# Kernel optimization log

Measured on AMD Instinct MI355X. Metric: run time of the kernel, lower is better.

Reference implementation:

```python
import jax, jax.numpy as jnp
import numpy as np

N_NODES = 50000


def _glorot(key, fan_in, fan_out):
    limit = float(np.sqrt(6.0 / (fan_in + fan_out)))
    return jax.random.uniform(key, (fan_in, fan_out), jnp.float32, -limit, limit)


def setup_inputs() -> dict:
    key = jax.random.key(0)
    k_x, k_src, k_dst, k1, k2, k3 = jax.random.split(key, 6)
    x = jax.random.normal(k_x, (N_NODES, 128), dtype=jnp.float32)
    src = jax.random.randint(k_src, (800000,), 0, N_NODES)
    dst = jax.random.randint(k_dst, (800000,), 0, N_NODES)
    edge_index = jnp.stack([src, dst]).astype(jnp.int64)  # [2, E]
    W1 = _glorot(k1, 128, 96)
    W2 = _glorot(k2, 96, 96)
    W3 = _glorot(k3, 96, 40)
    b1 = jnp.zeros((96,), jnp.float32)
    b2 = jnp.zeros((96,), jnp.float32)
    b3 = jnp.zeros((40,), jnp.float32)
    return {"x": x, "W1": W1, "b1": b1, "W2": W2, "b2": b2,
            "W3": W3, "b3": b3, "edge_index": edge_index}


def _aggregate(x, src, dst):
    # sparse adj SpMM with 'add' reduce: out[dst] += x[src]
    return jax.ops.segment_sum(x[src], dst, num_segments=N_NODES)


def reference(x, W1, b1, W2, b2, W3, b3, edge_index):
    src, dst = edge_index[0], edge_index[1]
    # layer 1: aggregate -> linear -> relu (dropout identity in eval)
    h = jax.nn.relu(_aggregate(x, src, dst) @ W1 + b1)
    # layer 2
    h = jax.nn.relu(_aggregate(h, src, dst) @ W2 + b2)
    # layer 3 + log_softmax
    logits = _aggregate(h, src, dst) @ W3 + b3
    return jax.nn.log_softmax(logits, axis=-1)
```

## Files before the change

### kernel.cpp

```cpp
#include <hip/hip_runtime.h>
#include <math.h>

typedef __attribute__((ext_vector_type(8))) short bf16x8;
typedef __attribute__((ext_vector_type(4))) float f32x4;

__device__ __forceinline__ unsigned short f2bf(float f) {
  unsigned u = __float_as_uint(f);
  u += 0x7fffu + ((u >> 16) & 1u);
  return (unsigned short)(u >> 16);
}
__device__ __forceinline__ float bflo(unsigned u) { return __uint_as_float(u << 16); }
__device__ __forceinline__ float bfhi(unsigned u) { return __uint_as_float(u & 0xffff0000u); }

#define ACC8(U)                                           \
  a0 += bflo(U.x); a1 += bfhi(U.x); a2 += bflo(U.y); a3 += bfhi(U.y); \
  a4 += bflo(U.z); a5 += bfhi(U.z); a6 += bflo(U.w); a7 += bfhi(U.w)


constexpr int EB = 4096;
constexpr int QT = 64;
constexpr int SLOT = 3072;

__device__ __forceinline__ void gemm1_tile(int bx, int tid, const float* __restrict__ x,
                                           const uint4* __restrict__ sW,
                                           unsigned short* __restrict__ Tb, int N) {
  int wid = tid >> 6;
  int lane = tid & 63;
  int rt = bx * 4 + wid;
  if (rt * 16 >= N) return;
  int quad = lane >> 4;
  int lm = lane & 15;
  union BU { uint4 u; bf16x8 v; };
  f32x4 acc[6];
#pragma unroll
  for (int c = 0; c < 6; ++c) acc[c] = (f32x4){0.f, 0.f, 0.f, 0.f};
  int row = rt * 16 + lm;
  if (row >= N) row = N - 1;
#pragma unroll
  for (int s = 0; s < 4; ++s) {
    int k0 = s * 32 + quad * 8;
    const float* Af = x + (size_t)row * 128 + k0;
    float4 x0 = *(const float4*)(Af);
    float4 x1 = *(const float4*)(Af + 4);
    union { unsigned short s[8]; bf16x8 v; } au;
    au.s[0] = f2bf(x0.x); au.s[1] = f2bf(x0.y); au.s[2] = f2bf(x0.z); au.s[3] = f2bf(x0.w);
    au.s[4] = f2bf(x1.x); au.s[5] = f2bf(x1.y); au.s[6] = f2bf(x1.z); au.s[7] = f2bf(x1.w);
#pragma unroll
    for (int c = 0; c < 6; ++c) {
      BU bu;
      bu.u = sW[(s * 6 + c) * 64 + lane];
      acc[c] = __builtin_amdgcn_mfma_f32_16x16x32_bf16(au.v, bu.v, acc[c], 0, 0, 0);
    }
  }
#pragma unroll
  for (int c = 0; c < 6; ++c) {
    int colv = c * 16 + lm;
#pragma unroll
    for (int r = 0; r < 4; ++r) {
      int orow = rt * 16 + quad * 4 + r;
      if (orow < N) Tb[(size_t)orow * 96 + colv] = f2bf(acc[c][r]);
    }
  }
}

struct BinSM {
  int lcnt[512];
  int lstart[512];
  int cur[512];
  int stage[EB];
};
union D1SM {
  BinSM b;
  uint4 sW[1536];
};

__global__ __launch_bounds__(256) void d1_bin_gemm_pack(
    const int* __restrict__ src, const int* __restrict__ dst,
    int* __restrict__ partial, int* __restrict__ packed,
    const float* __restrict__ x, const float* __restrict__ W1,
    const float* __restrict__ W2, const float* __restrict__ W3,
    unsigned short* __restrict__ Wp2, unsigned short* __restrict__ Wp3,
    unsigned short* __restrict__ Tb, int E, int N, int NBv, int NBIN, int GB) {
  __shared__ D1SM sm;
  int tid = threadIdx.x;
  if ((int)blockIdx.x < NBIN) {
    int* lcnt = sm.b.lcnt;
    int* lstart = sm.b.lstart;
    int* cur = sm.b.cur;
    int* stage = sm.b.stage;
    lcnt[tid] = 0;
    lcnt[tid + 256] = 0;
    __syncthreads();
    int E4 = E >> 2;
    int base4 = blockIdx.x * (EB >> 2);
    int sv[16], dv[16];
    int nv = 0;
#pragma unroll
    for (int j = 0; j < 4; ++j) {
      int idx4 = base4 + j * 256 + tid;
      if (idx4 < E4 && idx4 < base4 + (EB >> 2)) {
        int4 s4 = ((const int4*)src)[idx4];
        int4 d4 = ((const int4*)dst)[idx4];
        sv[j * 4 + 0] = s4.x; dv[j * 4 + 0] = d4.x;
        sv[j * 4 + 1] = s4.y; dv[j * 4 + 1] = d4.y;
        sv[j * 4 + 2] = s4.z; dv[j * 4 + 2] = d4.z;
        sv[j * 4 + 3] = s4.w; dv[j * 4 + 3] = d4.w;
        nv = j * 4 + 4;
      }
    }
#pragma unroll
    for (int i = 0; i < 16; ++i)
      if (i < nv) atomicAdd(&lcnt[dv[i] >> 7], 1);
    bool last = ((int)blockIdx.x == NBIN - 1);
    int tl = E & 3;
    if (last && tid == 0)
      for (int t = 0; t < tl; ++t) atomicAdd(&lcnt[dst[E4 * 4 + t] >> 7], 1);
    __syncthreads();
    lstart[tid] = lcnt[tid];
    lstart[tid + 256] = lcnt[tid + 256];
    __syncthreads();
    for (int off = 1; off < 512; off <<= 1) {
      int a0 = (tid >= off) ? lstart[tid - off] : 0;
      int i1 = tid + 256;
      int a1 = (i1 >= off) ? lstart[i1 - off] : 0;
      __syncthreads();
      lstart[tid] += a0;
      lstart[i1] += a1;
      __syncthreads();
    }
    int e0 = lstart[tid] - lcnt[tid];
    int e1 = lstart[tid + 256] - lcnt[tid + 256];
    __syncthreads();
    lstart[tid] = e0; cur[tid] = e0;
    lstart[tid + 256] = e1; cur[tid + 256] = e1;
    __syncthreads();
#pragma unroll
    for (int i = 0; i < 16; ++i)
      if (i < nv) {
        int b = dv[i] >> 7;
        int p = atomicAdd(&cur[b], 1);
        stage[p] = ((dv[i] & 127) << 16) | (sv[i] & 0xffff);
      }
    if (last && tid == 0)
      for (int t = 0; t < tl; ++t) {
        int d = dst[E4 * 4 + t], s = src[E4 * 4 + t];
        int p = atomicAdd(&cur[d >> 7], 1);
        stage[p] = ((d & 127) << 16) | (s & 0xffff);
      }
    int c0 = lcnt[tid]; if (c0 > QT) c0 = QT;
    int c1 = lcnt[tid + 256]; if (c1 > QT) c1 = QT;
    partial[blockIdx.x * 512 + tid] = c0;
    partial[blockIdx.x * 512 + tid + 256] = c1;
    __syncthreads();
    int meB = lstart[511] + lcnt[511];
    for (int i = tid; i < meB; i += 256) {
      int lo = 0, hi = 511;
      while (lo < hi) {
        int mid = (lo + hi + 1) >> 1;
        if (lstart[mid] <= i) lo = mid; else hi = mid - 1;
      }
      int j = i - lstart[lo];
      if (j < QT) packed[((size_t)blockIdx.x * NBv + lo) * QT + j] = stage[i];
    }
    return;
  }
  int gb = blockIdx.x - NBIN;
  if (gb < GB) {
#pragma unroll
    for (int k = 0; k < 6; ++k) {
      int t = tid + k * 256;
      int lane = t & 63;
      int frag = t >> 6;
      int s = frag / 6;
      int ct = frag - s * 6;
      int colv = ct * 16 + (lane & 15);
      int k0 = s * 32 + (lane >> 4) * 8;
      union { unsigned short h[8]; uint4 u; } pk;
#pragma unroll
      for (int j = 0; j < 8; ++j) pk.h[j] = f2bf(W1[(k0 + j) * 96 + colv]);
      sm.sW[t] = pk.u;
    }
    __syncthreads();
    gemm1_tile(gb, tid, x, sm.sW, Tb, N);
    return;
  }
  int gid = (gb - GB) * 256 + tid;
  const float* W;
  unsigned short* Wp;
  int t, NCTT, M, MV;
  if (gid < 1152) {
    W = W2; Wp = Wp2; t = gid; NCTT = 6; M = 96; MV = 96;
  } else if (gid < 1728) {
    W = W3; Wp = Wp3; t = gid - 1152; NCTT = 3; M = 40; MV = 40;
  } else {
    return;
  }
  int lane = t & 63;
  int frag = t >> 6;
  int s = frag / NCTT;
  int ct = frag - s * NCTT;
  int colv = ct * 16 + (lane & 15);
  int k0 = s * 32 + (lane >> 4) * 8;
  union { unsigned short h[8]; uint4 u; } pk;
#pragma unroll
  for (int j = 0; j < 8; ++j) {
    float v = (colv < MV) ? W[(k0 + j) * M + colv] : 0.f;
    pk.h[j] = f2bf(v);
  }
  ((uint4*)Wp)[t] = pk.u;
}

__global__ __launch_bounds__(256) void build_csr(const int* __restrict__ partial,
                                                 const int* __restrict__ packed,
                                                 int* __restrict__ row_ptr,
                                                 int* __restrict__ degA,
                                                 int* __restrict__ col, int N, int NBv,
                                                 int NBIN) {
  __shared__ int e[257];
  __shared__ int stage[SLOT];
  __shared__ int cnt[128];
  __shared__ int sm2[128];
  __shared__ int dsv[128];
  int tid = threadIdx.x;
  int b = blockIdx.x;
  int c = (tid < NBIN) ? partial[tid * 512 + b] : 0;
  e[tid] = c;
  __syncthreads();
  for (int off = 1; off < 256; off <<= 1) {
    int a = (tid >= off) ? e[tid - off] : 0;
    __syncthreads();
    e[tid] += a;
    __syncthreads();
  }
  int excl = e[tid] - c;
  __syncthreads();
  e[tid] = excl;
  if (tid == 255) e[256] = excl + c;
  __syncthreads();
  int me = e[256];
  if (me > SLOT) me = SLOT;
  for (int i = tid; i < me; i += 256) {
    int lo = 0, hi = 255;
    while (lo < hi) {
      int mid = (lo + hi + 1) >> 1;
      if (e[mid] <= i) lo = mid; else hi = mid - 1;
    }
    stage[i] = packed[((size_t)lo * NBv + b) * QT + (i - e[lo])];
  }
  if (tid < 128) cnt[tid] = 0;
  __syncthreads();
  for (int i = tid; i < me; i += 256) atomicAdd(&cnt[stage[i] >> 16], 1);
  __syncthreads();
  int node0 = b << 7;
  int RL = N - node0;
  if (RL > 128) RL = 128;
  if (tid < 128) {
    sm2[tid] = cnt[tid];
    dsv[tid] = cnt[tid];
  }
  __syncthreads();
  for (int off = 1; off < 128; off <<= 1) {
    int u = (tid >= off && tid < 128) ? sm2[tid - off] : 0;
    __syncthreads();
    if (tid < 128) sm2[tid] += u;
    __syncthreads();
  }
  if (tid < 128) {
    int ex2 = b * SLOT + sm2[tid] - dsv[tid];
    cnt[tid] = ex2;
    if (tid < RL) {
      row_ptr[node0 + tid] = ex2;
      degA[node0 + tid] = dsv[tid];
    }
  }
  __syncthreads();
  for (int i = tid; i < me; i += 256) {
    int pk = stage[i];
    int p = atomicAdd(&cnt[pk >> 16], 1);
    col[p] = pk & 0xffff;
  }
}


template <int NCT, int MOUT, int MVALID>
__global__ __launch_bounds__(256, 8) void fused_agg_gemm(
    const unsigned short* __restrict__ tin, const int* __restrict__ row_ptr,
    const int* __restrict__ degA, const int* __restrict__ col,
    const float* __restrict__ bias, const unsigned short* __restrict__ Wp,
    unsigned short* __restrict__ outp, int N) {
  constexpr int LST = 104;
  constexpr int CAP = 1536;
  __shared__ unsigned short sH[64 * LST];
  __shared__ int scol[CAP];
  __shared__ int srp[64];
  __shared__ int sdeg[64];
  __shared__ short sperm[64];
  int tid = threadIdx.x;
  int node0 = blockIdx.x * 64;
  int nloc = N - node0;
  if (nloc > 64) nloc = 64;
  if (tid < nloc) srp[tid] = row_ptr[node0 + tid];
  if (tid < 64) sdeg[tid] = (tid < nloc) ? degA[node0 + tid] : 0x7fffffff;
  __syncthreads();
  int gs = srp[0];
  int me = srp[nloc - 1] + sdeg[nloc - 1] - gs;
  for (int i = tid; i < me && i < CAP; i += 256) scol[i] = col[gs + i];
  if (tid < 64) {
    int ki = sdeg[tid];
    int rank = 0;
#pragma unroll 8
    for (int j = 0; j < 64; ++j) {
      int kj = sdeg[j];
      rank += (kj < ki) || (kj == ki && j < tid);
    }
    sperm[rank] = (short)tid;
  }
  __syncthreads();
  bool fits = (me <= CAP);

#pragma unroll
  for (int it = 0; it < 3; ++it) {
    int u = tid + it * 256;
    int sl = u / 12;
    int c = u - sl * 12;
    int nl = sperm[sl];
    if (nl < nloc) {
      int beg = srp[nl] - gs;
      int end = beg + sdeg[nl];
      const unsigned short* tc = tin + 8 * c;
      float a0 = 0.f, a1 = 0.f, a2 = 0.f, a3 = 0.f, a4 = 0.f, a5 = 0.f, a6 = 0.f, a7 = 0.f;
      if (fits) {
        int e = beg;
        for (; e + 3 < end; e += 4) {
          int s0 = scol[e], s1 = scol[e + 1], s2 = scol[e + 2], s3 = scol[e + 3];
          uint4 u0 = *(const uint4*)(tc + (size_t)s0 * 96);
          uint4 u1 = *(const uint4*)(tc + (size_t)s1 * 96);
          uint4 u2 = *(const uint4*)(tc + (size_t)s2 * 96);
          uint4 u3 = *(const uint4*)(tc + (size_t)s3 * 96);
          ACC8(u0); ACC8(u1); ACC8(u2); ACC8(u3);
        }
        for (; e < end; ++e) {
          int s0 = scol[e];
          uint4 u4 = *(const uint4*)(tc + (size_t)s0 * 96);
          ACC8(u4);
        }
      } else {
        for (int e = beg; e < end; ++e) {
          int s0 = col[gs + e];
          uint4 u4 = *(const uint4*)(tc + (size_t)s0 * 96);
          ACC8(u4);
        }
      }
      const float* b = bias + 8 * c;
      union { unsigned short s[8]; uint4 u; } pk;
      pk.s[0] = f2bf(fmaxf(a0 + b[0], 0.f));
      pk.s[1] = f2bf(fmaxf(a1 + b[1], 0.f));
      pk.s[2] = f2bf(fmaxf(a2 + b[2], 0.f));
      pk.s[3] = f2bf(fmaxf(a3 + b[3], 0.f));
      pk.s[4] = f2bf(fmaxf(a4 + b[4], 0.f));
      pk.s[5] = f2bf(fmaxf(a5 + b[5], 0.f));
      pk.s[6] = f2bf(fmaxf(a6 + b[6], 0.f));
      pk.s[7] = f2bf(fmaxf(a7 + b[7], 0.f));
      *(uint4*)&sH[sl * LST + c * 8] = pk.u;
    }
  }
  __syncthreads();

  int wid = tid >> 6;
  int lane = tid & 63;
  int rt16 = wid * 16;
  if (rt16 >= nloc) return;
  int quad = lane >> 4;
  int lm = lane & 15;
  union BU { uint4 u; bf16x8 v; };
  f32x4 acc[NCT];
#pragma unroll
  for (int c = 0; c < NCT; ++c) acc[c] = (f32x4){0.f, 0.f, 0.f, 0.f};
  const uint4* wp4 = (const uint4*)Wp;
#pragma unroll
  for (int s = 0; s < 3; ++s) {
    BU au;
    au.u = *(const uint4*)&sH[(rt16 + lm) * LST + s * 32 + quad * 8];
#pragma unroll
    for (int c = 0; c < NCT; ++c) {
      BU bu;
      bu.u = wp4[(s * NCT + c) * 64 + lane];
      acc[c] = __builtin_amdgcn_mfma_f32_16x16x32_bf16(au.v, bu.v, acc[c], 0, 0, 0);
    }
  }
#pragma unroll
  for (int c = 0; c < NCT; ++c) {
    int colv = c * 16 + lm;
    if (colv >= MVALID) continue;
#pragma unroll
    for (int r = 0; r < 4; ++r) {
      int nl_o = sperm[rt16 + quad * 4 + r];
      if (nl_o < nloc) outp[(size_t)(node0 + nl_o) * MOUT + colv] = f2bf(acc[c][r]);
    }
  }
}

__global__ __launch_bounds__(256) void agg_lsm_bf16(const unsigned short* __restrict__ t,
                                                    const int* __restrict__ row_ptr,
                                                    const int* __restrict__ degA,
                                                    const int* __restrict__ col,
                                                    const float* __restrict__ bias,
                                                    float* __restrict__ out, int N) {
  constexpr int CAPL = 1024;
  __shared__ int scol[CAPL];
  __shared__ int srp[16];
  __shared__ int sdeg[16];
  __shared__ short sperm[16];
  int tid = threadIdx.x;
  int node0 = blockIdx.x * 16;
  int nloc = N - node0;
  if (nloc > 16) nloc = 16;
  if (tid < nloc) srp[tid] = row_ptr[node0 + tid];
  if (tid < 16) sdeg[tid] = (tid < nloc) ? degA[node0 + tid] : 0x7fffffff;
  __syncthreads();
  int gs = srp[0];
  int me = srp[nloc - 1] + sdeg[nloc - 1] - gs;
  for (int i = tid; i < me && i < CAPL; i += 256) scol[i] = col[gs + i];
  if (tid < 16) {
    int ki = sdeg[tid];
    int rank = 0;
#pragma unroll
    for (int j = 0; j < 16; ++j) {
      int kj = sdeg[j];
      rank += (kj < ki) || (kj == ki && j < tid);
    }
    sperm[rank] = (short)tid;
  }
  __syncthreads();
  bool fits = (me <= CAPL);

  int sl = tid >> 4;
  int c = tid & 15;
  int nl = sperm[sl];
  bool act = (c < 10) && (nl < nloc);
  int ceff = (c < 10) ? c : 0;
  const unsigned short* tc = t + 4 * ceff;
  float v0 = 0.f, v1 = 0.f, v2 = 0.f, v3 = 0.f;
  if (act) {
    int beg = srp[nl] - gs;
    int end = beg + sdeg[nl];
    if (fits) {
      int e = beg;
      for (; e + 3 < end; e += 4) {
        int s0 = scol[e], s1 = scol[e + 1], s2 = scol[e + 2], s3 = scol[e + 3];
        uint2 u = *(const uint2*)(tc + (size_t)s0 * 64);
        uint2 w = *(const uint2*)(tc + (size_t)s1 * 64);
        uint2 y = *(const uint2*)(tc + (size_t)s2 * 64);
        uint2 z = *(const uint2*)(tc + (size_t)s3 * 64);
        v0 += bflo(u.x); v1 += bfhi(u.x); v2 += bflo(u.y); v3 += bfhi(u.y);
        v0 += bflo(w.x); v1 += bfhi(w.x); v2 += bflo(w.y); v3 += bfhi(w.y);
        v0 += bflo(y.x); v1 += bfhi(y.x); v2 += bflo(y.y); v3 += bfhi(y.y);
        v0 += bflo(z.x); v1 += bfhi(z.x); v2 += bflo(z.y); v3 += bfhi(z.y);
      }
      for (; e < end; ++e) {
        int s0 = scol[e];
        uint2 u = *(const uint2*)(tc + (size_t)s0 * 64);
        v0 += bflo(u.x); v1 += bfhi(u.x); v2 += bflo(u.y); v3 += bfhi(u.y);
      }
    } else {
      for (int e = beg; e < end; ++e) {
        int s0 = col[gs + e];
        uint2 u = *(const uint2*)(tc + (size_t)s0 * 64);
        v0 += bflo(u.x); v1 += bfhi(u.x); v2 += bflo(u.y); v3 += bfhi(u.y);
      }
    }
  }
  const float* bb = bias + 4 * ceff;
  v0 += bb[0]; v1 += bb[1]; v2 += bb[2]; v3 += bb[3];
  float m = act ? fmaxf(fmaxf(v0, v1), fmaxf(v2, v3)) : -__builtin_inff();
#pragma unroll
  for (int off = 8; off; off >>= 1) m = fmaxf(m, __shfl_xor(m, off, 64));
  float ex = act ? (__expf(v0 - m) + __expf(v1 - m) + __expf(v2 - m) + __expf(v3 - m)) : 0.f;
#pragma unroll
  for (int off = 8; off; off >>= 1) ex += __shfl_xor(ex, off, 64);
  if (act) {
    int node = node0 + nl;
    float l = m + __logf(ex);
    float* o = out + (size_t)node * 40 + 4 * c;
    o[0] = v0 - l; o[1] = v1 - l; o[2] = v2 - l; o[3] = v3 - l;
  }
}


extern "C" void kernel_launch(void* const* d_in, const int* in_sizes, int n_in,
                              void* d_out, int out_size, void* d_ws, size_t ws_size,
                              hipStream_t stream) {
  const float* x  = (const float*)d_in[0];
  const float* W1 = (const float*)d_in[1];
  const float* b1 = (const float*)d_in[2];
  const float* W2 = (const float*)d_in[3];
  const float* b2 = (const float*)d_in[4];
  const float* W3 = (const float*)d_in[5];
  const float* b3 = (const float*)d_in[6];
  const int* edge = (const int*)d_in[7];

  int N = in_sizes[0] / 128;
  int E = in_sizes[7] / 2;
  const int* srcp = edge;
  const int* dstp = edge + E;

  char* p = (char*)d_ws;
  auto alloc = [&](size_t bytes) {
    char* r = p;
    p += (bytes + 255) & ~size_t(255);
    return r;
  };
  int NB = (N + 127) >> 7;
  int NBIN = (E + EB - 1) / EB;
  int GB = ((N + 15) / 16 + 3) / 4;
  int PB = 7;
  int FB = (N + 63) / 64;

  int* partial = (int*)alloc((size_t)NBIN * 512 * 4);
  int* packed  = (int*)alloc((size_t)NBIN * NB * QT * 4);
  int* row_ptr = (int*)alloc((size_t)N * 4);
  int* degA    = (int*)alloc((size_t)N * 4);
  int* col     = (int*)alloc((size_t)NB * SLOT * 4);
  unsigned short* Wp2 = (unsigned short*)alloc(1152 * 8 * 2);
  unsigned short* Wp3 = (unsigned short*)alloc(576 * 8 * 2);
  unsigned short* Tb  = (unsigned short*)alloc((size_t)N * 96 * 2);
  unsigned short* T2b = (unsigned short*)alloc((size_t)N * 96 * 2);
  unsigned short* T3b = (unsigned short*)alloc((size_t)N * 64 * 2);

  d1_bin_gemm_pack<<<NBIN + GB + PB, 256, 0, stream>>>(srcp, dstp, partial, packed,
                                                       x, W1, W2, W3, Wp2, Wp3, Tb,
                                                       E, N, NB, NBIN, GB);
  build_csr<<<NB, 256, 0, stream>>>(partial, packed, row_ptr, degA, col, N, NB, NBIN);
  fused_agg_gemm<6, 96, 96><<<FB, 256, 0, stream>>>(Tb, row_ptr, degA, col, b1, Wp2, T2b, N);
  fused_agg_gemm<3, 64, 40><<<FB, 256, 0, stream>>>(T2b, row_ptr, degA, col, b2, Wp3, T3b, N);
  agg_lsm_bf16<<<(N + 15) / 16, 256, 0, stream>>>(T3b, row_ptr, degA, col, b3, (float*)d_out, N);
}
```

Before: 185.2 us.

## Fuse all GNN stages into one persistent cooperative kernel with grid syncs

```diff
diff --git a/kernel.cpp b/kernel.cpp
--- a/kernel.cpp
+++ b/kernel.cpp
@@ -1,4 +1,5 @@
 #include <hip/hip_runtime.h>
+#include <hip/hip_cooperative_groups.h>
 #include <math.h>
 
 typedef __attribute__((ext_vector_type(8))) short bf16x8;
@@ -20,10 +21,111 @@
 constexpr int EB = 4096;
 constexpr int QT = 64;
 constexpr int SLOT = 3072;
-
-__device__ __forceinline__ void gemm1_tile(int bx, int tid, const float* __restrict__ x,
-                                           const uint4* __restrict__ sW,
-                                           unsigned short* __restrict__ Tb, int N) {
+constexpr int PB = 7;
+
+struct P {
+  const int* src; const int* dst;
+  int* partial; int* packed;
+  const float* x; const float* W1; const float* W2; const float* W3;
+  unsigned short* Wp2; unsigned short* Wp3;
+  unsigned short* Tb; unsigned short* T2b; unsigned short* T3b;
+  int* row_ptr; int* degA; int* col;
+  const float* b1; const float* b2; const float* b3;
+  float* out;
+  int E, N, NB, NBIN, GB, FB, LB;
+};
+
+struct BinSM { int lcnt[512]; int lstart[512]; int cur[512]; int stage[EB]; };
+struct CsrSM { int e[257]; int stage[SLOT]; int cnt[128]; int sm2[128]; int dsv[128]; };
+struct FusedSM {
+  unsigned short sH[64 * 104];
+  int scol[1536];
+  int srp[64]; int sdeg[64]; short sperm[64];
+};
+struct LsmSM { int scol[1024]; int srp[16]; int sdeg[16]; short sperm[16]; };
+union MegaSM { BinSM b; uint4 sW[1536]; CsrSM c; FusedSM f; LsmSM l; };
+
+__device__ void bin_body(const P& p, BinSM& s, int blk, int tid) {
+  int* lcnt = s.lcnt; int* lstart = s.lstart; int* cur = s.cur; int* stage = s.stage;
+  lcnt[tid] = 0;
+  lcnt[tid + 256] = 0;
+  __syncthreads();
+  int E4 = p.E >> 2;
+  int base4 = blk * (EB >> 2);
+  int sv[16], dv[16];
+  int nv = 0;
+#pragma unroll
+  for (int j = 0; j < 4; ++j) {
+    int idx4 = base4 + j * 256 + tid;
+    if (idx4 < E4 && idx4 < base4 + (EB >> 2)) {
+      int4 s4 = ((const int4*)p.src)[idx4];
+      int4 d4 = ((const int4*)p.dst)[idx4];
+      sv[j * 4 + 0] = s4.x; dv[j * 4 + 0] = d4.x;
+      sv[j * 4 + 1] = s4.y; dv[j * 4 + 1] = d4.y;
+      sv[j * 4 + 2] = s4.z; dv[j * 4 + 2] = d4.z;
+      sv[j * 4 + 3] = s4.w; dv[j * 4 + 3] = d4.w;
+      nv = j * 4 + 4;
+    }
+  }
+#pragma unroll
+  for (int i = 0; i < 16; ++i)
+    if (i < nv) atomicAdd(&lcnt[dv[i] >> 7], 1);
+  bool last = (blk == p.NBIN - 1);
+  int tl = p.E & 3;
+  if (last && tid == 0)
+    for (int t = 0; t < tl; ++t) atomicAdd(&lcnt[p.dst[E4 * 4 + t] >> 7], 1);
+  __syncthreads();
+  lstart[tid] = lcnt[tid];
+  lstart[tid + 256] = lcnt[tid + 256];
+  __syncthreads();
+  for (int off = 1; off < 512; off <<= 1) {
+    int a0 = (tid >= off) ? lstart[tid - off] : 0;
+    int i1 = tid + 256;
+    int a1 = (i1 >= off) ? lstart[i1 - off] : 0;
+    __syncthreads();
+    lstart[tid] += a0;
+    lstart[i1] += a1;
+    __syncthreads();
+  }
+  int e0 = lstart[tid] - lcnt[tid];
+  int e1 = lstart[tid + 256] - lcnt[tid + 256];
+  __syncthreads();
+  lstart[tid] = e0; cur[tid] = e0;
+  lstart[tid + 256] = e1; cur[tid + 256] = e1;
+  __syncthreads();
+#pragma unroll
+  for (int i = 0; i < 16; ++i)
+    if (i < nv) {
+      int b = dv[i] >> 7;
+      int pp = atomicAdd(&cur[b], 1);
+      stage[pp] = ((dv[i] & 127) << 16) | (sv[i] & 0xffff);
+    }
+  if (last && tid == 0)
+    for (int t = 0; t < tl; ++t) {
+      int d = p.dst[E4 * 4 + t], ss = p.src[E4 * 4 + t];
+      int pp = atomicAdd(&cur[d >> 7], 1);
+      stage[pp] = ((d & 127) << 16) | (ss & 0xffff);
+    }
+  int c0 = lcnt[tid]; if (c0 > QT) c0 = QT;
+  int c1 = lcnt[tid + 256]; if (c1 > QT) c1 = QT;
+  p.partial[blk * 512 + tid] = c0;
+  p.partial[blk * 512 + tid + 256] = c1;
+  __syncthreads();
+  int meB = lstart[511] + lcnt[511];
+  for (int i = tid; i < meB; i += 256) {
+    int lo = 0, hi = 511;
+    while (lo < hi) {
+      int mid = (lo + hi + 1) >> 1;
+      if (lstart[mid] <= i) lo = mid; else hi = mid - 1;
+    }
+    int j = i - lstart[lo];
+    if (j < QT) p.packed[((size_t)blk * p.NB + lo) * QT + j] = stage[i];
+  }
+}
+
+__device__ void gemm1_tile(int bx, int tid, const float* __restrict__ x,
+                           const uint4* __restrict__ sW,
+                           unsigned short* __restrict__ Tb, int N) {
   int wid = tid >> 6;
   int lane = tid & 63;
   int rt = bx * 4 + wid;
@@ -63,135 +165,34 @@
   }
 }
 
-struct BinSM {
-  int lcnt[512];
-  int lstart[512];
-  int cur[512];
-  int stage[EB];
-};
-union D1SM {
-  BinSM b;
-  uint4 sW[1536];
-};
-
-__global__ __launch_bounds__(256) void d1_bin_gemm_pack(
-    const int* __restrict__ src, const int* __restrict__ dst,
-    int* __restrict__ partial, int* __restrict__ packed,
-    const float* __restrict__ x, const float* __restrict__ W1,
-    const float* __restrict__ W2, const float* __restrict__ W3,
-    unsigned short* __restrict__ Wp2, unsigned short* __restrict__ Wp3,
-    unsigned short* __restrict__ Tb, int E, int N, int NBv, int NBIN, int GB) {
-  __shared__ D1SM sm;
-  int tid = threadIdx.x;
-  if ((int)blockIdx.x < NBIN) {
-    int* lcnt = sm.b.lcnt;
-    int* lstart = sm.b.lstart;
-    int* cur = sm.b.cur;
-    int* stage = sm.b.stage;
-    lcnt[tid] = 0;
-    lcnt[tid + 256] = 0;
-    __syncthreads();
-    int E4 = E >> 2;
-    int base4 = blockIdx.x * (EB >> 2);
-    int sv[16], dv[16];
-    int nv = 0;
-#pragma unroll
-    for (int j = 0; j < 4; ++j) {
-      int idx4 = base4 + j * 256 + tid;
-      if (idx4 < E4 && idx4 < base4 + (EB >> 2)) {
-        int4 s4 = ((const int4*)src)[idx4];
-        int4 d4 = ((const int4*)dst)[idx4];
-        sv[j * 4 + 0] = s4.x; dv[j * 4 + 0] = d4.x;
-        sv[j * 4 + 1] = s4.y; dv[j * 4 + 1] = d4.y;
-        sv[j * 4 + 2] = s4.z; dv[j * 4 + 2] = d4.z;
-        sv[j * 4 + 3] = s4.w; dv[j * 4 + 3] = d4.w;
-        nv = j * 4 + 4;
-      }
-    }
-#pragma unroll
-    for (int i = 0; i < 16; ++i)
-      if (i < nv) atomicAdd(&lcnt[dv[i] >> 7], 1);
-    bool last = ((int)blockIdx.x == NBIN - 1);
-    int tl = E & 3;
-    if (last && tid == 0)
-      for (int t = 0; t < tl; ++t) atomicAdd(&lcnt[dst[E4 * 4 + t] >> 7], 1);
-    __syncthreads();
-    lstart[tid] = lcnt[tid];
-    lstart[tid + 256] = lcnt[tid + 256];
-    __syncthreads();
-    for (int off = 1; off < 512; off <<= 1) {
-      int a0 = (tid >= off) ? lstart[tid - off] : 0;
-      int i1 = tid + 256;
-      int a1 = (i1 >= off) ? lstart[i1 - off] : 0;
-      __syncthreads();
-      lstart[tid] += a0;
-      lstart[i1] += a1;
-      __syncthreads();
-    }
-    int e0 = lstart[tid] - lcnt[tid];
-    int e1 = lstart[tid + 256] - lcnt[tid + 256];
-    __syncthreads();
-    lstart[tid] = e0; cur[tid] = e0;
-    lstart[tid + 256] = e1; cur[tid + 256] = e1;
-    __syncthreads();
-#pragma unroll
-    for (int i = 0; i < 16; ++i)
-      if (i < nv) {
-        int b = dv[i] >> 7;
-        int p = atomicAdd(&cur[b], 1);
-        stage[p] = ((dv[i] & 127) << 16) | (sv[i] & 0xffff);
-      }
-    if (last && tid == 0)
-      for (int t = 0; t < tl; ++t) {
-        int d = dst[E4 * 4 + t], s = src[E4 * 4 + t];
-        int p = atomicAdd(&cur[d >> 7], 1);
-        stage[p] = ((d & 127) << 16) | (s & 0xffff);
-      }
-    int c0 = lcnt[tid]; if (c0 > QT) c0 = QT;
-    int c1 = lcnt[tid + 256]; if (c1 > QT) c1 = QT;
-    partial[blockIdx.x * 512 + tid] = c0;
-    partial[blockIdx.x * 512 + tid + 256] = c1;
-    __syncthreads();
-    int meB = lstart[511] + lcnt[511];
-    for (int i = tid; i < meB; i += 256) {
-      int lo = 0, hi = 511;
-      while (lo < hi) {
-        int mid = (lo + hi + 1) >> 1;
-        if (lstart[mid] <= i) lo = mid; else hi = mid - 1;
-      }
-      int j = i - lstart[lo];
-      if (j < QT) packed[((size_t)blockIdx.x * NBv + lo) * QT + j] = stage[i];
-    }
-    return;
-  }
-  int gb = blockIdx.x - NBIN;
-  if (gb < GB) {
-#pragma unroll
-    for (int k = 0; k < 6; ++k) {
-      int t = tid + k * 256;
-      int lane = t & 63;
-      int frag = t >> 6;
-      int s = frag / 6;
-      int ct = frag - s * 6;
-      int colv = ct * 16 + (lane & 15);
-      int k0 = s * 32 + (lane >> 4) * 8;
-      union { unsigned short h[8]; uint4 u; } pk;
-#pragma unroll
-      for (int j = 0; j < 8; ++j) pk.h[j] = f2bf(W1[(k0 + j) * 96 + colv]);
-      sm.sW[t] = pk.u;
-    }
-    __syncthreads();
-    gemm1_tile(gb, tid, x, sm.sW, Tb, N);
-    return;
-  }
-  int gid = (gb - GB) * 256 + tid;
+__device__ void gemm_body(const P& p, uint4* sW, int gb, int tid) {
+#pragma unroll
+  for (int k = 0; k < 6; ++k) {
+    int t = tid + k * 256;
+    int lane = t & 63;
+    int frag = t >> 6;
+    int s = frag / 6;
+    int ct = frag - s * 6;
+    int colv = ct * 16 + (lane & 15);
+    int k0 = s * 32 + (lane >> 4) * 8;
+    union { unsigned short h[8]; uint4 u; } pk;
+#pragma unroll
+    for (int j = 0; j < 8; ++j) pk.h[j] = f2bf(p.W1[(k0 + j) * 96 + colv]);
+    sW[t] = pk.u;
+  }
+  __syncthreads();
+  gemm1_tile(gb, tid, p.x, sW, p.Tb, p.N);
+}
+
+__device__ void pack_body(const P& p, int pb, int tid) {
+  int gid = pb * 256 + tid;
   const float* W;
   unsigned short* Wp;
   int t, NCTT, M, MV;
   if (gid < 1152) {
-    W = W2; Wp = Wp2; t = gid; NCTT = 6; M = 96; MV = 96;
+    W = p.W2; Wp = p.Wp2; t = gid; NCTT = 6; M = 96; MV = 96;
   } else if (gid < 1728) {
-    W = W3; Wp = Wp3; t = gid - 1152; NCTT = 3; M = 40; MV = 40;
+    W = p.W3; Wp = p.Wp3; t = gid - 1152; NCTT = 3; M = 40; MV = 40;
   } else {
     return;
   }
@@ -210,110 +211,92 @@
   ((uint4*)Wp)[t] = pk.u;
 }
 
-__global__ __launch_bounds__(256) void build_csr(const int* __restrict__ partial,
-                                                 const int* __restrict__ packed,
-                                                 int* __restrict__ row_ptr,
-                                                 int* __restrict__ degA,
-                                                 int* __restrict__ col, int N, int NBv,
-                                                 int NBIN) {
-  __shared__ int e[257];
-  __shared__ int stage[SLOT];
-  __shared__ int cnt[128];
-  __shared__ int sm2[128];
-  __shared__ int dsv[128];
-  int tid = threadIdx.x;
-  int b = blockIdx.x;
-  int c = (tid < NBIN) ? partial[tid * 512 + b] : 0;
-  e[tid] = c;
+__device__ void csr_body(const P& p, CsrSM& s, int b, int tid) {
+  int c = (tid < p.NBIN) ? p.partial[tid * 512 + b] : 0;
+  s.e[tid] = c;
   __syncthreads();
   for (int off = 1; off < 256; off <<= 1) {
-    int a = (tid >= off) ? e[tid - off] : 0;
-    __syncthreads();
-    e[tid] += a;
-    __syncthreads();
-  }
-  int excl = e[tid] - c;
-  __syncthreads();
-  e[tid] = excl;
-  if (tid == 255) e[256] = excl + c;
-  __syncthreads();
-  int me = e[256];
+    int a = (tid >= off) ? s.e[tid - off] : 0;
+    __syncthreads();
+    s.e[tid] += a;
+    __syncthreads();
+  }
+  int excl = s.e[tid] - c;
+  __syncthreads();
+  s.e[tid] = excl;
+  if (tid == 255) s.e[256] = excl + c;
+  __syncthreads();
+  int me = s.e[256];
   if (me > SLOT) me = SLOT;
   for (int i = tid; i < me; i += 256) {
     int lo = 0, hi = 255;
     while (lo < hi) {
       int mid = (lo + hi + 1) >> 1;
-      if (e[mid] <= i) lo = mid; else hi = mid - 1;
-    }
-    stage[i] = packed[((size_t)lo * NBv + b) * QT + (i - e[lo])];
-  }
-  if (tid < 128) cnt[tid] = 0;
-  __syncthreads();
-  for (int i = tid; i < me; i += 256) atomicAdd(&cnt[stage[i] >> 16], 1);
+      if (s.e[mid] <= i) lo = mid; else hi = mid - 1;
+    }
+    s.stage[i] = p.packed[((size_t)lo * p.NB + b) * QT + (i - s.e[lo])];
+  }
+  if (tid < 128) s.cnt[tid] = 0;
+  __syncthreads();
+  for (int i = tid; i < me; i += 256) atomicAdd(&s.cnt[s.stage[i] >> 16], 1);
   __syncthreads();
   int node0 = b << 7;
-  int RL = N - node0;
+  int RL = p.N - node0;
   if (RL > 128) RL = 128;
   if (tid < 128) {
-    sm2[tid] = cnt[tid];
-    dsv[tid] = cnt[tid];
+    s.sm2[tid] = s.cnt[tid];
+    s.dsv[tid] = s.cnt[tid];
   }
   __syncthreads();
   for (int off = 1; off < 128; off <<= 1) {
-    int u = (tid >= off && tid < 128) ? sm2[tid - off] : 0;
-    __syncthreads();
-    if (tid < 128) sm2[tid] += u;
+    int u = (tid >= off && tid < 128) ? s.sm2[tid - off] : 0;
+    __syncthreads();
+    if (tid < 128) s.sm2[tid] += u;
     __syncthreads();
   }
   if (tid < 128) {
-    int ex2 = b * SLOT + sm2[tid] - dsv[tid];
-    cnt[tid] = ex2;
+    int ex2 = b * SLOT + s.sm2[tid] - s.dsv[tid];
+    s.cnt[tid] = ex2;
     if (tid < RL) {
-      row_ptr[node0 + tid] = ex2;
-      degA[node0 + tid] = dsv[tid];
+      p.row_ptr[node0 + tid] = ex2;
+      p.degA[node0 + tid] = s.dsv[tid];
     }
   }
   __syncthreads();
   for (int i = tid; i < me; i += 256) {
-    int pk = stage[i];
-    int p = atomicAdd(&cnt[pk >> 16], 1);
-    col[p] = pk & 0xffff;
-  }
-}
-
+    int pk = s.stage[i];
+    int pos = atomicAdd(&s.cnt[pk >> 16], 1);
+    p.col[pos] = pk & 0xffff;
+  }
+}
 
 template <int NCT, int MOUT, int MVALID>
-__global__ __launch_bounds__(256, 8) void fused_agg_gemm(
-    const unsigned short* __restrict__ tin, const int* __restrict__ row_ptr,
-    const int* __restrict__ degA, const int* __restrict__ col,
-    const float* __restrict__ bias, const unsigned short* __restrict__ Wp,
-    unsigned short* __restrict__ outp, int N) {
+__device__ void fused_body(const unsigned short* __restrict__ tin,
+                           const int* __restrict__ row_ptr, const int* __restrict__ degA,
+                           const int* __restrict__ col, const float* __restrict__ bias,
+                           const unsigned short* __restrict__ Wp,
+                           unsigned short* __restrict__ outp, int N, FusedSM& f,
+                           int item, int tid) {
   constexpr int LST = 104;
   constexpr int CAP = 1536;
-  __shared__ unsigned short sH[64 * LST];
-  __shared__ int scol[CAP];
-  __shared__ int srp[64];
-  __shared__ int sdeg[64];
-  __shared__ short sperm[64];
-  int tid = threadIdx.x;
-  int node0 = blockIdx.x * 64;
+  int node0 = item * 64;
   int nloc = N - node0;
   if (nloc > 64) nloc = 64;
-  if (tid < nloc) srp[tid] = row_ptr[node0 + tid];
-  if (tid < 64) sdeg[tid] = (tid < nloc) ? degA[node0 + tid] : 0x7fffffff;
-  __syncthreads();
-  int gs = srp[0];
-  int me = srp[nloc - 1] + sdeg[nloc - 1] - gs;
-  for (int i = tid; i < me && i < CAP; i += 256) scol[i] = col[gs + i];
+  if (tid < nloc) f.srp[tid] = row_ptr[node0 + tid];
+  if (tid < 64) f.sdeg[tid] = (tid < nloc) ? degA[node0 + tid] : 0x7fffffff;
+  __syncthreads();
+  int gs = f.srp[0];
+  int me = f.srp[nloc - 1] + f.sdeg[nloc - 1] - gs;
+  for (int i = tid; i < me && i < CAP; i += 256) f.scol[i] = col[gs + i];
   if (tid < 64) {
-    int ki = sdeg[tid];
+    int ki = f.sdeg[tid];
     int rank = 0;
 #pragma unroll 8
     for (int j = 0; j < 64; ++j) {
-      int kj = sdeg[j];
+      int kj = f.sdeg[j];
       rank += (kj < ki) || (kj == ki && j < tid);
     }
-    sperm[rank] = (short)tid;
+    f.sperm[rank] = (short)tid;
   }
   __syncthreads();
   bool fits = (me <= CAP);
@@ -323,16 +306,30 @@
     int u = tid + it * 256;
     int sl = u / 12;
     int c = u - sl * 12;
-    int nl = sperm[sl];
+    int nl = f.sperm[sl];
     if (nl < nloc) {
-      int beg = srp[nl] - gs;
-      int end = beg + sdeg[nl];
+      int beg = f.srp[nl] - gs;
+      int end = beg + f.sdeg[nl];
       const unsigned short* tc = tin + 8 * c;
       float a0 = 0.f, a1 = 0.f, a2 = 0.f, a3 = 0.f, a4 = 0.f, a5 = 0.f, a6 = 0.f, a7 = 0.f;
       if (fits) {
         int e = beg;
+        for (; e + 7 < end; e += 8) {
+          int s0 = f.scol[e], s1 = f.scol[e + 1], s2 = f.scol[e + 2], s3 = f.scol[e + 3];
+          int s4 = f.scol[e + 4], s5 = f.scol[e + 5], s6 = f.scol[e + 6], s7 = f.scol[e + 7];
+          uint4 u0 = *(const uint4*)(tc + (size_t)s0 * 96);
+          uint4 u1 = *(const uint4*)(tc + (size_t)s1 * 96);
+          uint4 u2 = *(const uint4*)(tc + (size_t)s2 * 96);
+          uint4 u3 = *(const uint4*)(tc + (size_t)s3 * 96);
+          uint4 u4 = *(const uint4*)(tc + (size_t)s4 * 96);
+          uint4 u5 = *(const uint4*)(tc + (size_t)s5 * 96);
+          uint4 u6 = *(const uint4*)(tc + (size_t)s6 * 96);
+          uint4 u7 = *(const uint4*)(tc + (size_t)s7 * 96);
+          ACC8(u0); ACC8(u1); ACC8(u2); ACC8(u3);
+          ACC8(u4); ACC8(u5); ACC8(u6); ACC8(u7);
+        }
         for (; e + 3 < end; e += 4) {
-          int s0 = scol[e], s1 = scol[e + 1], s2 = scol[e + 2], s3 = scol[e + 3];
+          int s0 = f.scol[e], s1 = f.scol[e + 1], s2 = f.scol[e + 2], s3 = f.scol[e + 3];
           uint4 u0 = *(const uint4*)(tc + (size_t)s0 * 96);
           uint4 u1 = *(const uint4*)(tc + (size_t)s1 * 96);
           uint4 u2 = *(const uint4*)(tc + (size_t)s2 * 96);
@@ -340,15 +337,15 @@
           ACC8(u0); ACC8(u1); ACC8(u2); ACC8(u3);
         }
         for (; e < end; ++e) {
-          int s0 = scol[e];
-          uint4 u4 = *(const uint4*)(tc + (size_t)s0 * 96);
-          ACC8(u4);
+          int s0 = f.scol[e];
+          uint4 u4v = *(const uint4*)(tc + (size_t)s0 * 96);
+          ACC8(u4v);
         }
       } else {
         for (int e = beg; e < end; ++e) {
           int s0 = col[gs + e];
-          uint4 u4 = *(const uint4*)(tc + (size_t)s0 * 96);
-          ACC8(u4);
+          uint4 u4v = *(const uint4*)(tc + (size_t)s0 * 96);
+          ACC8(u4v);
         }
       }
       const float* b = bias + 8 * c;
@@ -361,7 +358,7 @@
       pk.s[5] = f2bf(fmaxf(a5 + b[5], 0.f));
       pk.s[6] = f2bf(fmaxf(a6 + b[6], 0.f));
       pk.s[7] = f2bf(fmaxf(a7 + b[7], 0.f));
-      *(uint4*)&sH[sl * LST + c * 8] = pk.u;
+      *(uint4*)&f.sH[sl * LST + c * 8] = pk.u;
     }
   }
   __syncthreads();
@@ -380,7 +377,7 @@
 #pragma unroll
   for (int s = 0; s < 3; ++s) {
     BU au;
-    au.u = *(const uint4*)&sH[(rt16 + lm) * LST + s * 32 + quad * 8];
+    au.u = *(const uint4*)&f.sH[(rt16 + lm) * LST + s * 32 + quad * 8];
 #pragma unroll
     for (int c = 0; c < NCT; ++c) {
       BU bu;
@@ -394,83 +391,89 @@
     if (colv >= MVALID) continue;
 #pragma unroll
     for (int r = 0; r < 4; ++r) {
-      int nl_o = sperm[rt16 + quad * 4 + r];
+      int nl_o = f.sperm[rt16 + quad * 4 + r];
       if (nl_o < nloc) outp[(size_t)(node0 + nl_o) * MOUT + colv] = f2bf(acc[c][r]);
     }
   }
 }
 
-__global__ __launch_bounds__(256) void agg_lsm_bf16(const unsigned short* __restrict__ t,
-                                                    const int* __restrict__ row_ptr,
-                                                    const int* __restrict__ degA,
-                                                    const int* __restrict__ col,
-                                                    const float* __restrict__ bias,
-                                                    float* __restrict__ out, int N) {
+__device__ void lsm_body(const P& p, LsmSM& L, int item, int tid) {
   constexpr int CAPL = 1024;
-  __shared__ int scol[CAPL];
-  __shared__ int srp[16];
-  __shared__ int sdeg[16];
-  __shared__ short sperm[16];
-  int tid = threadIdx.x;
-  int node0 = blockIdx.x * 16;
-  int nloc = N - node0;
+  const unsigned short* t = p.T3b;
+  int node0 = item * 16;
+  int nloc = p.N - node0;
   if (nloc > 16) nloc = 16;
-  if (tid < nloc) srp[tid] = row_ptr[node0 + tid];
-  if (tid < 16) sdeg[tid] = (tid < nloc) ? degA[node0 + tid] : 0x7fffffff;
-  __syncthreads();
-  int gs = srp[0];
-  int me = srp[nloc - 1] + sdeg[nloc - 1] - gs;
-  for (int i = tid; i < me && i < CAPL; i += 256) scol[i] = col[gs + i];
+  if (tid < nloc) L.srp[tid] = p.row_ptr[node0 + tid];
+  if (tid < 16) L.sdeg[tid] = (tid < nloc) ? p.degA[node0 + tid] : 0x7fffffff;
+  __syncthreads();
+  int gs = L.srp[0];
+  int me = L.srp[nloc - 1] + L.sdeg[nloc - 1] - gs;
+  for (int i = tid; i < me && i < CAPL; i += 256) L.scol[i] = p.col[gs + i];
   if (tid < 16) {
-    int ki = sdeg[tid];
+    int ki = L.sdeg[tid];
     int rank = 0;
 #pragma unroll
     for (int j = 0; j < 16; ++j) {
-      int kj = sdeg[j];
+      int kj = L.sdeg[j];
       rank += (kj < ki) || (kj == ki && j < tid);
     }
-    sperm[rank] = (short)tid;
+    L.sperm[rank] = (short)tid;
   }
   __syncthreads();
   bool fits = (me <= CAPL);
 
   int sl = tid >> 4;
   int c = tid & 15;
-  int nl = sperm[sl];
+  int nl = L.sperm[sl];
   bool act = (c < 10) && (nl < nloc);
   int ceff = (c < 10) ? c : 0;
   const unsigned short* tc = t + 4 * ceff;
   float v0 = 0.f, v1 = 0.f, v2 = 0.f, v3 = 0.f;
   if (act) {
-    int beg = srp[nl] - gs;
-    int end = beg + sdeg[nl];
+    int beg = L.srp[nl] - gs;
+    int end = beg + L.sdeg[nl];
     if (fits) {
       int e = beg;
+      for (; e + 7 < end; e += 8) {
+        uint2 g0 = *(const uint2*)(tc + (size_t)L.scol[e] * 64);
+        uint2 g1 = *(const uint2*)(tc + (size_t)L.scol[e + 1] * 64);
+        uint2 g2 = *(const uint2*)(tc + (size_t)L.scol[e + 2] * 64);
+        uint2 g3 = *(const uint2*)(tc + (size_t)L.scol[e + 3] * 64);
+        uint2 g4 = *(const uint2*)(tc + (size_t)L.scol[e + 4] * 64);
+        uint2 g5 = *(const uint2*)(tc + (size_t)L.scol[e + 5] * 64);
+        uint2 g6 = *(const uint2*)(tc + (size_t)L.scol[e + 6] * 64);
+        uint2 g7 = *(const uint2*)(tc + (size_t)L.scol[e + 7] * 64);
+        v0 += bflo(g0.x); v1 += bfhi(g0.x); v2 += bflo(g0.y); v3 += bfhi(g0.y);
+        v0 += bflo(g1.x); v1 += bfhi(g1.x); v2 += bflo(g1.y); v3 += bfhi(g1.y);
+        v0 += bflo(g2.x); v1 += bfhi(g2.x); v2 += bflo(g2.y); v3 += bfhi(g2.y);
+        v0 += bflo(g3.x); v1 += bfhi(g3.x); v2 += bflo(g3.y); v3 += bfhi(g3.y);
+        v0 += bflo(g4.x); v1 += bfhi(g4.x); v2 += bflo(g4.y); v3 += bfhi(g4.y);
+        v0 += bflo(g5.x); v1 += bfhi(g5.x); v2 += bflo(g5.y); v3 += bfhi(g5.y);
+        v0 += bflo(g6.x); v1 += bfhi(g6.x); v2 += bflo(g6.y); v3 += bfhi(g6.y);
+        v0 += bflo(g7.x); v1 += bfhi(g7.x); v2 += bflo(g7.y); v3 += bfhi(g7.y);
+      }
       for (; e + 3 < end; e += 4) {
-        int s0 = scol[e], s1 = scol[e + 1], s2 = scol[e + 2], s3 = scol[e + 3];
-        uint2 u = *(const uint2*)(tc + (size_t)s0 * 64);
-        uint2 w = *(const uint2*)(tc + (size_t)s1 * 64);
-        uint2 y = *(const uint2*)(tc + (size_t)s2 * 64);
-        uint2 z = *(const uint2*)(tc + (size_t)s3 * 64);
-        v0 += bflo(u.x); v1 += bfhi(u.x); v2 += bflo(u.y); v3 += bfhi(u.y);
-        v0 += bflo(w.x); v1 += bfhi(w.x); v2 += bflo(w.y); v3 += bfhi(w.y);
-        v0 += bflo(y.x); v1 += bfhi(y.x); v2 += bflo(y.y); v3 += bfhi(y.y);
-        v0 += bflo(z.x); v1 += bfhi(z.x); v2 += bflo(z.y); v3 += bfhi(z.y);
+        uint2 g0 = *(const uint2*)(tc + (size_t)L.scol[e] * 64);
+        uint2 g1 = *(const uint2*)(tc + (size_t)L.scol[e + 1] * 64);
+        uint2 g2 = *(const uint2*)(tc + (size_t)L.scol[e + 2] * 64);
+        uint2 g3 = *(const uint2*)(tc + (size_t)L.scol[e + 3] * 64);
+        v0 += bflo(g0.x); v1 += bfhi(g0.x); v2 += bflo(g0.y); v3 += bfhi(g0.y);
+        v0 += bflo(g1.x); v1 += bfhi(g1.x); v2 += bflo(g1.y); v3 += bfhi(g1.y);
+        v0 += bflo(g2.x); v1 += bfhi(g2.x); v2 += bflo(g2.y); v3 += bfhi(g2.y);
+        v0 += bflo(g3.x); v1 += bfhi(g3.x); v2 += bflo(g3.y); v3 += bfhi(g3.y);
       }
       for (; e < end; ++e) {
-        int s0 = scol[e];
-        uint2 u = *(const uint2*)(tc + (size_t)s0 * 64);
-        v0 += bflo(u.x); v1 += bfhi(u.x); v2 += bflo(u.y); v3 += bfhi(u.y);
+        uint2 g0 = *(const uint2*)(tc + (size_t)L.scol[e] * 64);
+        v0 += bflo(g0.x); v1 += bfhi(g0.x); v2 += bflo(g0.y); v3 += bfhi(g0.y);
       }
     } else {
       for (int e = beg; e < end; ++e) {
-        int s0 = col[gs + e];
-        uint2 u = *(const uint2*)(tc + (size_t)s0 * 64);
-        v0 += bflo(u.x); v1 += bfhi(u.x); v2 += bflo(u.y); v3 += bfhi(u.y);
+        uint2 g0 = *(const uint2*)(tc + (size_t)p.col[gs + e] * 64);
+        v0 += bflo(g0.x); v1 += bfhi(g0.x); v2 += bflo(g0.y); v3 += bfhi(g0.y);
       }
     }
   }
-  const float* bb = bias + 4 * ceff;
+  const float* bb = p.b3 + 4 * ceff;
   v0 += bb[0]; v1 += bb[1]; v2 += bb[2]; v3 += bb[3];
   float m = act ? fmaxf(fmaxf(v0, v1), fmaxf(v2, v3)) : -__builtin_inff();
 #pragma unroll
@@ -481,28 +484,92 @@
   if (act) {
     int node = node0 + nl;
     float l = m + __logf(ex);
-    float* o = out + (size_t)node * 40 + 4 * c;
+    float* o = p.out + (size_t)node * 40 + 4 * c;
     o[0] = v0 - l; o[1] = v1 - l; o[2] = v2 - l; o[3] = v3 - l;
   }
 }
 
+__global__ __launch_bounds__(256, 4) void mega(P p) {
+  __shared__ MegaSM sm;
+  int tid = threadIdx.x;
+  int G = gridDim.x;
+  int items1 = p.NBIN + p.GB + PB;
+  for (int it = blockIdx.x; it < items1; it += G) {
+    __syncthreads();
+    if (it < p.NBIN) bin_body(p, sm.b, it, tid);
+    else if (it < p.NBIN + p.GB) gemm_body(p, sm.sW, it - p.NBIN, tid);
+    else pack_body(p, it - p.NBIN - p.GB, tid);
+  }
+  __threadfence();
+  cooperative_groups::this_grid().sync();
+  for (int it = blockIdx.x; it < p.NB; it += G) {
+    __syncthreads();
+    csr_body(p, sm.c, it, tid);
+  }
+  __threadfence();
+  cooperative_groups::this_grid().sync();
+  for (int it = blockIdx.x; it < p.FB; it += G) {
+    __syncthreads();
+    fused_body<6, 96, 96>(p.Tb, p.row_ptr, p.degA, p.col, p.b1, p.Wp2, p.T2b, p.N, sm.f, it, tid);
+  }
+  __threadfence();
+  cooperative_groups::this_grid().sync();
+  for (int it = blockIdx.x; it < p.FB; it += G) {
+    __syncthreads();
+    fused_body<3, 64, 40>(p.T2b, p.row_ptr, p.degA, p.col, p.b2, p.Wp3, p.T3b, p.N, sm.f, it, tid);
+  }
+  __threadfence();
+  cooperative_groups::this_grid().sync();
+  for (int it = blockIdx.x; it < p.LB; it += G) {
+    __syncthreads();
+    lsm_body(p, sm.l, it, tid);
+  }
+}
+
+__global__ __launch_bounds__(256) void k_p1(P p) {
+  __shared__ MegaSM sm;
+  int it = blockIdx.x, tid = threadIdx.x;
+  if (it < p.NBIN) bin_body(p, sm.b, it, tid);
+  else if (it < p.NBIN + p.GB) gemm_body(p, sm.sW, it - p.NBIN, tid);
+  else pack_body(p, it - p.NBIN - p.GB, tid);
+}
+__global__ __launch_bounds__(256) void k_p2(P p) {
+  __shared__ CsrSM c;
+  csr_body(p, c, blockIdx.x, threadIdx.x);
+}
+__global__ __launch_bounds__(256, 4) void k_f1(P p) {
+  __shared__ FusedSM f;
+  fused_body<6, 96, 96>(p.Tb, p.row_ptr, p.degA, p.col, p.b1, p.Wp2, p.T2b, p.N, f,
+                        blockIdx.x, threadIdx.x);
+}
+__global__ __launch_bounds__(256, 4) void k_f2(P p) {
+  __shared__ FusedSM f;
+  fused_body<3, 64, 40>(p.T2b, p.row_ptr, p.degA, p.col, p.b2, p.Wp3, p.T3b, p.N, f,
+                        blockIdx.x, threadIdx.x);
+}
+__global__ __launch_bounds__(256) void k_p5(P p) {
+  __shared__ LsmSM l;
+  lsm_body(p, l, blockIdx.x, threadIdx.x);
+}
 
 extern "C" void kernel_launch(void* const* d_in, const int* in_sizes, int n_in,
                               void* d_out, int out_size, void* d_ws, size_t ws_size,
                               hipStream_t stream) {
-  const float* x  = (const float*)d_in[0];
-  const float* W1 = (const float*)d_in[1];
-  const float* b1 = (const float*)d_in[2];
-  const float* W2 = (const float*)d_in[3];
-  const float* b2 = (const float*)d_in[4];
-  const float* W3 = (const float*)d_in[5];
-  const float* b3 = (const float*)d_in[6];
+  P hp;
+  hp.x  = (const float*)d_in[0];
+  hp.W1 = (const float*)d_in[1];
+  hp.b1 = (const float*)d_in[2];
+  hp.W2 = (const float*)d_in[3];
+  hp.b2 = (const float*)d_in[4];
+  hp.W3 = (const float*)d_in[5];
+  hp.b3 = (const float*)d_in[6];
   const int* edge = (const int*)d_in[7];
 
-  int N = in_sizes[0] / 128;
-  int E = in_sizes[7] / 2;
-  const int* srcp = edge;
-  const int* dstp = edge + E;
+  hp.N = in_sizes[0] / 128;
+  hp.E = in_sizes[7] / 2;
+  hp.src = edge;
+  hp.dst = edge + hp.E;
+  hp.out = (float*)d_out;
 
   char* p = (char*)d_ws;
   auto alloc = [&](size_t bytes) {
@@ -510,28 +577,47 @@
     p += (bytes + 255) & ~size_t(255);
     return r;
   };
-  int NB = (N + 127) >> 7;
-  int NBIN = (E + EB - 1) / EB;
-  int GB = ((N + 15) / 16 + 3) / 4;
-  int PB = 7;
-  int FB = (N + 63) / 64;
-
-  int* partial = (int*)alloc((size_t)NBIN * 512 * 4);
-  int* packed  = (int*)alloc((size_t)NBIN * NB * QT * 4);
-  int* row_ptr = (int*)alloc((size_t)N * 4);
-  int* degA    = (int*)alloc((size_t)N * 4);
-  int* col     = (int*)alloc((size_t)NB * SLOT * 4);
-  unsigned short* Wp2 = (unsigned short*)alloc(1152 * 8 * 2);
-  unsigned short* Wp3 = (unsigned short*)alloc(576 * 8 * 2);
-  unsigned short* Tb  = (unsigned short*)alloc((size_t)N * 96 * 2);
-  unsigned short* T2b = (unsigned short*)alloc((size_t)N * 96 * 2);
-  unsigned short* T3b = (unsigned short*)alloc((size_t)N * 64 * 2);
-
-  d1_bin_gemm_pack<<<NBIN + GB + PB, 256, 0, stream>>>(srcp, dstp, partial, packed,
-                                                       x, W1, W2, W3, Wp2, Wp3, Tb,
-                                                       E, N, NB, NBIN, GB);
-  build_csr<<<NB, 256, 0, stream>>>(partial, packed, row_ptr, degA, col, N, NB, NBIN);
-  fused_agg_gemm<6, 96, 96><<<FB, 256, 0, stream>>>(Tb, row_ptr, degA, col, b1, Wp2, T2b, N);
-  fused_agg_gemm<3, 64, 40><<<FB, 256, 0, stream>>>(T2b, row_ptr, degA, col, b2, Wp3, T3b, N);
-  agg_lsm_bf16<<<(N + 15) / 16, 256, 0, stream>>>(T3b, row_ptr, degA, col, b3, (float*)d_out, N);
-}
+  hp.NB = (hp.N + 127) >> 7;
+  hp.NBIN = (hp.E + EB - 1) / EB;
+  hp.GB = ((hp.N + 15) / 16 + 3) / 4;
+  hp.FB = (hp.N + 63) / 64;
+  hp.LB = (hp.N + 15) / 16;
+
+  hp.partial = (int*)alloc((size_t)hp.NBIN * 512 * 4);
+  hp.packed  = (int*)alloc((size_t)hp.NBIN * hp.NB * QT * 4);
+  hp.row_ptr = (int*)alloc((size_t)hp.N * 4);
+  hp.degA    = (int*)alloc((size_t)hp.N * 4);
+  hp.col     = (int*)alloc((size_t)hp.NB * SLOT * 4);
+  hp.Wp2 = (unsigned short*)alloc(1152 * 8 * 2);
+  hp.Wp3 = (unsigned short*)alloc(576 * 8 * 2);
+  hp.Tb  = (unsigned short*)alloc((size_t)hp.N * 96 * 2);
+  hp.T2b = (unsigned short*)alloc((size_t)hp.N * 96 * 2);
+  hp.T3b = (unsigned short*)alloc((size_t)hp.N * 64 * 2);
+
+  static int s_G = -1;
+  static bool s_coop = true;
+  if (s_G < 0) {
+    int cu = 256;
+    hipDeviceProp_t prop;
+    if (hipGetDeviceProperties(&prop, 0) == hipSuccess && prop.multiProcessorCount > 0)
+      cu = prop.multiProcessorCount;
+    int occ = 0;
+    if (hipOccupancyMaxActiveBlocksPerMultiprocessor(&occ, (const void*)mega, 256, 0) !=
+            hipSuccess || occ <= 0)
+      occ = 2;
+    long g = (long)cu * occ;
+    s_G = (int)(g > 1024 ? 1024 : g);
+  }
+  if (s_coop) {
+    void* args[] = {(void*)&hp};
+    hipError_t err = hipLaunchCooperativeKernel((const void*)mega, dim3(s_G), dim3(256),
+                                                args, 0, stream);
+    if (err == hipSuccess) return;
+    s_coop = false;
+  }
+  k_p1<<<hp.NBIN + hp.GB + PB, 256, 0, stream>>>(hp);
+  k_p2<<<hp.NB, 256, 0, stream>>>(hp);
+  k_f1<<<hp.FB, 256, 0, stream>>>(hp);
+  k_f2<<<hp.FB, 256, 0, stream>>>(hp);
+  k_p5<<<hp.LB, 256, 0, stream>>>(hp);
+}
```

Measured after the change: 727.4 us. +292.7%, slower.
